# Kernel tuning notes

Measured on AMD Instinct MI355X. Metric: run time of the kernel, lower is better.

The kernel has to match this reference:

```python
import jax, jax.numpy as jnp
import numpy as np

E, H, I, K, T = 8, 1024, 2816, 2, 2048


def setup_inputs() -> dict:
    key = jax.random.key(0)
    k1, k2, k3, k4, k5, k6 = jax.random.split(key, 6)
    hidden_states = jax.random.normal(k1, (T, H), dtype=jnp.float32)
    top_k_indices = jax.random.randint(k2, (T, K), 0, E, dtype=jnp.int32)
    raw = jax.random.uniform(k3, (T, K), dtype=jnp.float32) + 0.1
    top_k_values = raw / jnp.sum(raw, axis=-1, keepdims=True)  # router softmax-like weights
    scale = 1.0 / np.sqrt(H)
    w_gate = jax.random.normal(k4, (E, H, I), dtype=jnp.float32) * scale
    w_up = jax.random.normal(k5, (E, H, I), dtype=jnp.float32) * scale
    w_down = jax.random.normal(k6, (E, I, H), dtype=jnp.float32) * (1.0 / np.sqrt(I))
    return {
        "hidden_states": hidden_states,
        "top_k_indices": top_k_indices,
        "top_k_values": top_k_values,
        "w_gate": w_gate,
        "w_up": w_up,
        "w_down": w_down,
    }


def reference(hidden_states, top_k_indices, top_k_values, w_gate, w_up, w_down):
    # Each expert: SwiGLU FFN  down( silu(x @ gate) * (x @ up) )
    # Run every expert on every token (dense reference for grouped-GEMM dispatch),
    # then combine with the per-token top-k routing weights.
    def expert(wg, wu, wd):
        g = jnp.matmul(hidden_states, wg)          # [T, I]
        u = jnp.matmul(hidden_states, wu)          # [T, I]
        return jnp.matmul(jax.nn.silu(g) * u, wd)  # [T, H]

    y = jax.vmap(expert)(w_gate, w_up, w_down)     # [E, T, H]

    t = hidden_states.shape[0]
    # comb[t, e] = sum over k of top_k_values[t, k] where top_k_indices[t, k] == e
    comb = jnp.zeros((t, w_gate.shape[0]), dtype=hidden_states.dtype)
    comb = comb.at[jnp.arange(t)[:, None], top_k_indices].add(top_k_values)
    out = jnp.einsum('te,eth->th', comb, y)        # weighted combine -> [T, H]
    return out
```

## Files before the change

### kernel.cpp

```cpp
#include <hip/hip_runtime.h>
#include <stdint.h>

#define T_TOK 2048
#define KTOP  2
#define NEXP  8
#define HDIM  1024
#define IDIM  2816

#define NPAIR 4096

#define BM        128
#define MAX_TILES 40
#define NPP       (NPAIR + BM)
#define BN2       128
#define BK2       32
#define BN3       64
#define BK3       64

#define R1BM   256
#define R1T    24
#define R1NPP  (NPAIR + R1BM)
#define R1BN2  128
#define R1BK2  32
#define R1BKp2 40
#define R1BN3  64
#define R1BK3  64
#define R1BKp3 72

typedef __attribute__((ext_vector_type(8))) short short8;
typedef __attribute__((ext_vector_type(4))) float floatx4;

__device__ __forceinline__ unsigned short f2bf(float f) {
  unsigned int u = __float_as_uint(f);
  u += 0x7fffu + ((u >> 16) & 1u);
  return (unsigned short)(u >> 16);
}

__device__ __forceinline__ void glds16(const unsigned short* g, unsigned short* l) {
  __builtin_amdgcn_global_load_lds(
      (const __attribute__((address_space(1))) unsigned int*)g,
      (__attribute__((address_space(3))) unsigned int*)l, 16, 0, 0);
}

__global__ void setup_kernel(const int* __restrict__ idx,
                             const float* __restrict__ vals,
                             int* __restrict__ hdr,
                             int* __restrict__ stok,
                             float* __restrict__ sw, int bm) {
  __shared__ int cnt[NEXP];
  __shared__ int off[NEXP];
  int tid = threadIdx.x;
  if (tid < NEXP) cnt[tid] = 0;
  __syncthreads();
  for (int p = tid; p < NPAIR; p += blockDim.x) atomicAdd(&cnt[idx[p]], 1);
  __syncthreads();
  if (tid == 0) {
    int s = 0, nt = 0;
    for (int e = 0; e < NEXP; ++e) {
      off[e] = s;
      int n = cnt[e];
      for (int t0 = 0; t0 < n; t0 += bm) {
        hdr[nt] = e;
        hdr[64 + nt] = s + t0;
        hdr[128 + nt] = s + n;
        nt++;
      }
      s += n;
    }
    for (; nt < 64; ++nt) hdr[nt] = -1;
  }
  __syncthreads();
  for (int p = tid; p < NPAIR; p += blockDim.x) {
    int e = idx[p];
    int pos = atomicAdd(&off[e], 1);
    stok[pos] = p / KTOP;
    sw[pos] = vals[p];
  }
}

__global__ void gather_kernel(const float* __restrict__ hidden,
                              const int* __restrict__ stok,
                              unsigned short* __restrict__ Xs) {
  int p = blockIdx.x;
  int t = stok[p];
  const float4* src = reinterpret_cast<const float4*>(hidden + (size_t)t * HDIM);
  float4 v = src[threadIdx.x];
  uint2 q;
  q.x = f2bf(v.x) | ((unsigned)f2bf(v.y) << 16);
  q.y = f2bf(v.z) | ((unsigned)f2bf(v.w) << 16);
  *reinterpret_cast<uint2*>(Xs + (size_t)p * HDIM + threadIdx.x * 4) = q;
}

__global__ __launch_bounds__(256) void convert_kernel(
    const float* __restrict__ wg, const float* __restrict__ wu,
    const float* __restrict__ wd, unsigned short* __restrict__ wgT,
    unsigned short* __restrict__ wuT, unsigned short* __restrict__ wdT,
    int zoff) {
  __shared__ float ls[64][65];
  int z = blockIdx.z + zoff;
  int e = blockIdx.y;
  int M = (z == 2) ? IDIM : HDIM;
  int N = (z == 2) ? HDIM : IDIM;
  const float* src = (z == 0 ? wg : z == 1 ? wu : wd) + (size_t)e * M * N;
  unsigned short* dst = (z == 0 ? wgT : z == 1 ? wuT : wdT) + (size_t)e * M * N;
  int ntx = N >> 6;
  int n0 = (blockIdx.x % ntx) << 6;
  int m0 = (blockIdx.x / ntx) << 6;
  int t = threadIdx.x;
  int rr = t >> 4, cc = (t & 15) * 4;
#pragma unroll
  for (int i = 0; i < 4; ++i) {
    int r = rr + i * 16;
    float4 v = *reinterpret_cast<const float4*>(src + (size_t)(m0 + r) * N + n0 + cc);
    ls[r][cc] = v.x; ls[r][cc + 1] = v.y; ls[r][cc + 2] = v.z; ls[r][cc + 3] = v.w;
  }
  __syncthreads();
  int mc = (t & 7) * 8, nn = t >> 3;
#pragma unroll
  for (int i = 0; i < 2; ++i) {
    int n = nn + i * 32;
    uint4 q;
    q.x = f2bf(ls[mc][n])     | ((unsigned)f2bf(ls[mc + 1][n]) << 16);
    q.y = f2bf(ls[mc + 2][n]) | ((unsigned)f2bf(ls[mc + 3][n]) << 16);
    q.z = f2bf(ls[mc + 4][n]) | ((unsigned)f2bf(ls[mc + 5][n]) << 16);
    q.w = f2bf(ls[mc + 6][n]) | ((unsigned)f2bf(ls[mc + 7][n]) << 16);
    *reinterpret_cast<uint4*>(dst + (size_t)(n0 + n) * M + m0 + mc) = q;
  }
}

__global__ __launch_bounds__(256, 2) void gateup_kernel(
    const unsigned short* __restrict__ Xs, const unsigned short* __restrict__ wgT,
    const unsigned short* __restrict__ wuT, const int* __restrict__ hdr,
    const float* __restrict__ sw_g, unsigned short* __restrict__ Act) {
  int bx = blockIdx.x;
  int e = hdr[bx];
  if (e < 0) return;
  int row0 = hdr[64 + bx];
  int rowlim = hdr[128 + bx] - row0;
  int n0 = blockIdx.y * BN2;

  __shared__ __align__(16) unsigned short As[BM * BK2];
  __shared__ __align__(16) unsigned short Bg[BN2 * BK2];
  __shared__ __align__(16) unsigned short Bu[BN2 * BK2];
  __shared__ float sw[BM];

  int tid = threadIdx.x, lane = tid & 63, wave = tid >> 6;
  if (tid < BM) sw[tid] = sw_g[row0 + tid];

  const unsigned short* wgb = wgT + (size_t)e * IDIM * HDIM;
  const unsigned short* wub = wuT + (size_t)e * IDIM * HDIM;

  floatx4 accg[4][4], accu[4][4];
  floatx4 zz = {0.f, 0.f, 0.f, 0.f};
#pragma unroll
  for (int a = 0; a < 4; ++a)
#pragma unroll
    for (int b = 0; b < 4; ++b) { accg[a][b] = zz; accu[a][b] = zz; }

  int wm = (wave >> 1) * 64, wn = (wave & 1) * 64;
  int lr = lane >> 2;
  int lk = (((lane & 3) ^ ((lr >> 1) & 3)) * 8);
  int fr = lane & 15;
  int fq = (((lane >> 4) ^ ((fr >> 1) & 3)) * 8);

  for (int kb = 0; kb < HDIM; kb += BK2) {
#pragma unroll
    for (int it = 0; it < 2; ++it) {
      int c = wave * 2 + it;
      glds16(Xs  + (size_t)(row0 + c * 16 + lr) * HDIM + kb + lk, &As[c * 512]);
      glds16(wgb + (size_t)(n0  + c * 16 + lr) * HDIM + kb + lk, &Bg[c * 512]);
      glds16(wub + (size_t)(n0  + c * 16 + lr) * HDIM + kb + lk, &Bu[c * 512]);
    }
    __syncthreads();

    short8 af[4], bg8[4], bu8[4];
#pragma unroll
    for (int x = 0; x < 4; ++x) {
      af[x]  = *reinterpret_cast<const short8*>(&As[(wm + x * 16 + fr) * BK2 + fq]);
      bg8[x] = *reinterpret_cast<const short8*>(&Bg[(wn + x * 16 + fr) * BK2 + fq]);
      bu8[x] = *reinterpret_cast<const short8*>(&Bu[(wn + x * 16 + fr) * BK2 + fq]);
    }
#pragma unroll
    for (int tm = 0; tm < 4; ++tm)
#pragma unroll
      for (int tn = 0; tn < 4; ++tn) {
        accg[tm][tn] = __builtin_amdgcn_mfma_f32_16x16x32_bf16(af[tm], bg8[tn], accg[tm][tn], 0, 0, 0);
        accu[tm][tn] = __builtin_amdgcn_mfma_f32_16x16x32_bf16(af[tm], bu8[tn], accu[tm][tn], 0, 0, 0);
      }
    __syncthreads();
  }

#pragma unroll
  for (int tm = 0; tm < 4; ++tm)
#pragma unroll
    for (int tn = 0; tn < 4; ++tn)
#pragma unroll
      for (int r = 0; r < 4; ++r) {
        int rl = wm + tm * 16 + (lane >> 4) * 4 + r;
        if (rl < rowlim) {
          int col = n0 + wn + tn * 16 + fr;
          float g = accg[tm][tn][r];
          float u = accu[tm][tn][r];
          float s = g / (1.f + __expf(-g));
          Act[(size_t)(row0 + rl) * IDIM + col] = f2bf(s * u * sw[rl]);
        }
      }
}

__global__ __launch_bounds__(256, 3) void down_kernel(
    const unsigned short* __restrict__ Act, const unsigned short* __restrict__ wdT,
    const int* __restrict__ hdr, const int* __restrict__ stok,
    float* __restrict__ out) {
  int bx = blockIdx.x;
  int e = hdr[bx];
  if (e < 0) return;
  int row0 = hdr[64 + bx];
  int rowlim = hdr[128 + bx] - row0;
  int n0 = blockIdx.y * BN3;

  __shared__ __align__(16) unsigned short As[BM * BK3];
  __shared__ __align__(16) unsigned short Bd[BN3 * BK3];
  __shared__ int stk[BM];

  int tid = threadIdx.x, lane = tid & 63, wave = tid >> 6;
  if (tid < BM) stk[tid] = stok[row0 + tid];

  const unsigned short* wdb = wdT + (size_t)e * HDIM * IDIM;

  floatx4 acc[4][2];
  floatx4 zz = {0.f, 0.f, 0.f, 0.f};
#pragma unroll
  for (int a = 0; a < 4; ++a) { acc[a][0] = zz; acc[a][1] = zz; }

  int wm = (wave >> 1) * 64, wn = (wave & 1) * 32;
  int lr8 = lane >> 3;
  int lk8 = (((lane & 7) ^ lr8) * 8);
  int fr = lane & 15;
  int fk = fr & 7;

  for (int kb = 0; kb < IDIM; kb += BK3) {
#pragma unroll
    for (int it = 0; it < 4; ++it) {
      int c = wave * 4 + it;
      glds16(Act + (size_t)(row0 + c * 8 + lr8) * IDIM + kb + lk8, &As[c * 512]);
    }
#pragma unroll
    for (int it = 0; it < 2; ++it) {
      int c = wave * 2 + it;
      glds16(wdb + (size_t)(n0 + c * 8 + lr8) * IDIM + kb + lk8, &Bd[c * 512]);
    }
    __syncthreads();

#pragma unroll
    for (int ks = 0; ks < BK3; ks += 32) {
      int q8 = (ks >> 3) + (lane >> 4);
      int fo = ((q8 ^ fk) * 8);
      short8 af[4], bd8[2];
#pragma unroll
      for (int x = 0; x < 4; ++x)
        af[x] = *reinterpret_cast<const short8*>(&As[(wm + x * 16 + fr) * BK3 + fo]);
#pragma unroll
      for (int x = 0; x < 2; ++x)
        bd8[x] = *reinterpret_cast<const short8*>(&Bd[(wn + x * 16 + fr) * BK3 + fo]);
#pragma unroll
      for (int tm = 0; tm < 4; ++tm)
#pragma unroll
        for (int tn = 0; tn < 2; ++tn)
          acc[tm][tn] = __builtin_amdgcn_mfma_f32_16x16x32_bf16(af[tm], bd8[tn], acc[tm][tn], 0, 0, 0);
    }
    __syncthreads();
  }

#pragma unroll
  for (int tm = 0; tm < 4; ++tm)
#pragma unroll
    for (int tn = 0; tn < 2; ++tn)
#pragma unroll
      for (int r = 0; r < 4; ++r) {
        int rl = wm + tm * 16 + (lane >> 4) * 4 + r;
        if (rl < rowlim) {
          int col = n0 + wn + tn * 16 + fr;
          unsafeAtomicAdd(&out[(size_t)stk[rl] * HDIM + col], acc[tm][tn][r]);
        }
      }
}

__global__ __launch_bounds__(512, 2) void gateup_fb(
    const unsigned short* __restrict__ Xs, const float* __restrict__ wg,
    const float* __restrict__ wu, const int* __restrict__ hdr,
    const float* __restrict__ sw_g, unsigned short* __restrict__ Act) {
  int by = blockIdx.y;
  int e = hdr[by];
  if (e < 0) return;
  int row0 = hdr[64 + by];
  int row_end = hdr[128 + by];
  int n0 = blockIdx.x * R1BN2;

  __shared__ __align__(16) unsigned short As[R1BM * R1BKp2];
  __shared__ __align__(16) unsigned short Bg[R1BN2 * R1BKp2];
  __shared__ __align__(16) unsigned short Bu[R1BN2 * R1BKp2];
  __shared__ float sw[R1BM];

  int tid = threadIdx.x, lane = tid & 63, wave = tid >> 6;
  if (tid < R1BM) sw[tid] = sw_g[row0 + tid];

  const float* wgb = wg + (size_t)e * HDIM * IDIM;
  const float* wub = wu + (size_t)e * HDIM * IDIM;

  floatx4 accg[4][4], accu[4][4];
  floatx4 zz = {0.f, 0.f, 0.f, 0.f};
#pragma unroll
  for (int a = 0; a < 4; ++a)
#pragma unroll
    for (int b = 0; b < 4; ++b) { accg[a][b] = zz; accu[a][b] = zz; }

  int wm = (wave >> 1) * 64, wn = (wave & 1) * 64;

  for (int kb = 0; kb < HDIM; kb += R1BK2) {
    __syncthreads();
#pragma unroll
    for (int it = 0; it < 2; ++it) {
      int cc = wave * 2 + it;
      int m = cc * 16 + (lane >> 2);
      int k = (lane & 3) * 8;
      uint4 v = *reinterpret_cast<const uint4*>(Xs + (size_t)(row0 + m) * HDIM + kb + k);
      *reinterpret_cast<uint4*>(&As[m * R1BKp2 + k]) = v;
    }
#pragma unroll
    for (int it = 0; it < 2; ++it) {
      int cc = wave * 2 + it;
      const float* wb = (cc & 8) ? wub : wgb;
      unsigned short* Bs = (cc & 8) ? Bu : Bg;
      int r = cc & 7;
      int kblk = r >> 1, nh = r & 1;
      int n = nh * 64 + lane;
      int k = kblk * 8;
      const float* src = wb + (size_t)(kb + k) * IDIM + n0 + n;
      uint4 q;
      q.x = f2bf(src[0])                | ((unsigned)f2bf(src[(size_t)IDIM])     << 16);
      q.y = f2bf(src[2 * (size_t)IDIM]) | ((unsigned)f2bf(src[3 * (size_t)IDIM]) << 16);
      q.z = f2bf(src[4 * (size_t)IDIM]) | ((unsigned)f2bf(src[5 * (size_t)IDIM]) << 16);
      q.w = f2bf(src[6 * (size_t)IDIM]) | ((unsigned)f2bf(src[7 * (size_t)IDIM]) << 16);
      *reinterpret_cast<uint4*>(&Bs[n * R1BKp2 + k]) = q;
    }
    __syncthreads();

    int krd = (lane >> 4) * 8;
    short8 af[4], bgf[4], buf_[4];
#pragma unroll
    for (int tm = 0; tm < 4; ++tm)
      af[tm] = *reinterpret_cast<const short8*>(&As[(wm + tm * 16 + (lane & 15)) * R1BKp2 + krd]);
#pragma unroll
    for (int tn = 0; tn < 4; ++tn) {
      bgf[tn]  = *reinterpret_cast<const short8*>(&Bg[(wn + tn * 16 + (lane & 15)) * R1BKp2 + krd]);
      buf_[tn] = *reinterpret_cast<const short8*>(&Bu[(wn + tn * 16 + (lane & 15)) * R1BKp2 + krd]);
    }
#pragma unroll
    for (int tm = 0; tm < 4; ++tm)
#pragma unroll
      for (int tn = 0; tn < 4; ++tn) {
        accg[tm][tn] = __builtin_amdgcn_mfma_f32_16x16x32_bf16(af[tm], bgf[tn], accg[tm][tn], 0, 0, 0);
        accu[tm][tn] = __builtin_amdgcn_mfma_f32_16x16x32_bf16(af[tm], buf_[tn], accu[tm][tn], 0, 0, 0);
      }
  }

  int rowlim = row_end - row0;
#pragma unroll
  for (int tm = 0; tm < 4; ++tm)
#pragma unroll
    for (int tn = 0; tn < 4; ++tn)
#pragma unroll
      for (int r = 0; r < 4; ++r) {
        int rl = wm + tm * 16 + (lane >> 4) * 4 + r;
        if (rl < rowlim) {
          int col = n0 + wn + tn * 16 + (lane & 15);
          float g = accg[tm][tn][r];
          float u = accu[tm][tn][r];
          float s = g / (1.f + __expf(-g));
          Act[(size_t)(row0 + rl) * IDIM + col] = f2bf(s * u * sw[rl]);
        }
      }
}

__global__ __launch_bounds__(512, 2) void down_fb(
    const unsigned short* __restrict__ Act, const float* __restrict__ wd,
    const int* __restrict__ hdr, const int* __restrict__ stok,
    float* __restrict__ out) {
  int by = blockIdx.y;
  int e = hdr[by];
  if (e < 0) return;
  int row0 = hdr[64 + by];
  int row_end = hdr[128 + by];
  int n0 = blockIdx.x * R1BN3;

  __shared__ __align__(16) unsigned short As[R1BM * R1BKp3];
  __shared__ __align__(16) unsigned short Bd[R1BN3 * R1BKp3];
  __shared__ int stk[R1BM];

  int tid = threadIdx.x, lane = tid & 63, wave = tid >> 6;
  if (tid < R1BM) stk[tid] = stok[row0 + tid];

  const float* wdb = wd + (size_t)e * IDIM * HDIM;

  floatx4 acc[4][2];
  floatx4 zz = {0.f, 0.f, 0.f, 0.f};
#pragma unroll
  for (int a = 0; a < 4; ++a) { acc[a][0] = zz; acc[a][1] = zz; }

  int wm = (wave >> 1) * 64, wn = (wave & 1) * 32;

  for (int kb = 0; kb < IDIM; kb += R1BK3) {
    __syncthreads();
#pragma unroll
    for (int it = 0; it < 4; ++it) {
      int cc = wave * 4 + it;
      int m = cc * 8 + (lane >> 3);
      int k = (lane & 7) * 8;
      uint4 v = *reinterpret_cast<const uint4*>(Act + (size_t)(row0 + m) * IDIM + kb + k);
      *reinterpret_cast<uint4*>(&As[m * R1BKp3 + k]) = v;
    }
    {
      int n = lane;
      int k = wave * 8;
      const float* src = wdb + (size_t)(kb + k) * HDIM + n0 + n;
      uint4 q;
      q.x = f2bf(src[0])        | ((unsigned)f2bf(src[HDIM])     << 16);
      q.y = f2bf(src[2 * HDIM]) | ((unsigned)f2bf(src[3 * HDIM]) << 16);
      q.z = f2bf(src[4 * HDIM]) | ((unsigned)f2bf(src[5 * HDIM]) << 16);
      q.w = f2bf(src[6 * HDIM]) | ((unsigned)f2bf(src[7 * HDIM]) << 16);
      *reinterpret_cast<uint4*>(&Bd[n * R1BKp3 + k]) = q;
    }
    __syncthreads();

#pragma unroll
    for (int ks = 0; ks < R1BK3; ks += 32) {
      int krd = ks + (lane >> 4) * 8;
      short8 af[4], bdf[2];
#pragma unroll
      for (int tm = 0; tm < 4; ++tm)
        af[tm] = *reinterpret_cast<const short8*>(&As[(wm + tm * 16 + (lane & 15)) * R1BKp3 + krd]);
#pragma unroll
      for (int tn = 0; tn < 2; ++tn)
        bdf[tn] = *reinterpret_cast<const short8*>(&Bd[(wn + tn * 16 + (lane & 15)) * R1BKp3 + krd]);
#pragma unroll
      for (int tm = 0; tm < 4; ++tm)
#pragma unroll
        for (int tn = 0; tn < 2; ++tn)
          acc[tm][tn] = __builtin_amdgcn_mfma_f32_16x16x32_bf16(af[tm], bdf[tn], acc[tm][tn], 0, 0, 0);
    }
  }

  int rowlim = row_end - row0;
#pragma unroll
  for (int tm = 0; tm < 4; ++tm)
#pragma unroll
    for (int tn = 0; tn < 2; ++tn)
#pragma unroll
      for (int r = 0; r < 4; ++r) {
        int rl = wm + tm * 16 + (lane >> 4) * 4 + r;
        if (rl < rowlim) {
          int col = n0 + wn + tn * 16 + (lane & 15);
          unsafeAtomicAdd(&out[(size_t)stk[rl] * HDIM + col], acc[tm][tn][r]);
        }
      }
}

extern "C" void kernel_launch(void* const* d_in, const int* in_sizes, int n_in,
                              void* d_out, int out_size, void* d_ws, size_t ws_size,
                              hipStream_t stream) {
  const float* hidden = (const float*)d_in[0];
  const int* idx = (const int*)d_in[1];
  const float* vals = (const float*)d_in[2];
  const float* wg = (const float*)d_in[3];
  const float* wu = (const float*)d_in[4];
  const float* wd = (const float*)d_in[5];
  float* out = (float*)d_out;
  char* ws = (char*)d_ws;

  hipMemsetAsync(d_out, 0, (size_t)out_size * sizeof(float), stream);

  const size_t OFF_STOK = 4096;
  const size_t OFF_SW   = OFF_STOK + (size_t)NPP * 4;
  const size_t OFF_XS   = 65536;
  const size_t OFF_ACT  = OFF_XS + (size_t)NPP * HDIM * 2;
  const size_t OFF_WG   = OFF_ACT + (size_t)NPP * IDIM * 2;
  const size_t WSZ      = (size_t)NEXP * HDIM * IDIM * 2;
  const size_t OFF_WU   = OFF_WG + WSZ;
  const size_t NEED     = OFF_WU + WSZ;

  if (ws_size >= NEED) {
    int* hdr = (int*)ws;
    int* stok = (int*)(ws + OFF_STOK);
    float* sw = (float*)(ws + OFF_SW);
    unsigned short* Xs  = (unsigned short*)(ws + OFF_XS);
    unsigned short* Act = (unsigned short*)(ws + OFF_ACT);
    unsigned short* wgT = (unsigned short*)(ws + OFF_WG);
    unsigned short* wuT = (unsigned short*)(ws + OFF_WU);
    unsigned short* wdT = wgT;

    setup_kernel<<<1, 256, 0, stream>>>(idx, vals, hdr, stok, sw, BM);
    convert_kernel<<<dim3(704, NEXP, 2), 256, 0, stream>>>(wg, wu, wd, wgT, wuT, wdT, 0);
    gather_kernel<<<NPAIR, 256, 0, stream>>>(hidden, stok, Xs);
    gateup_kernel<<<dim3(MAX_TILES, IDIM / BN2), 256, 0, stream>>>(Xs, wgT, wuT, hdr, sw, Act);
    convert_kernel<<<dim3(704, NEXP, 1), 256, 0, stream>>>(wg, wu, wd, wgT, wuT, wdT, 2);
    down_kernel<<<dim3(MAX_TILES, HDIM / BN3), 256, 0, stream>>>(Act, wdT, hdr, stok, out);
  } else {
    int* hdr = (int*)ws;
    int* stok = (int*)(ws + 4096);
    float* sw = (float*)(ws + 4096 + (size_t)R1NPP * 4);
    unsigned short* Xs  = (unsigned short*)(ws + 65536);
    unsigned short* Act = (unsigned short*)(ws + 65536 + (size_t)R1NPP * HDIM * 2);

    setup_kernel<<<1, 256, 0, stream>>>(idx, vals, hdr, stok, sw, R1BM);
    gather_kernel<<<NPAIR, 256, 0, stream>>>(hidden, stok, Xs);
    gateup_fb<<<dim3(IDIM / R1BN2, R1T), 512, 0, stream>>>(Xs, wg, wu, hdr, sw, Act);
    down_fb<<<dim3(HDIM / R1BN3, R1T), 512, 0, stream>>>(Act, wd, hdr, stok, out);
  }
}
```

Baseline: 451.8 us.

## Double-buffer LDS in grouped GEMMs, remap tiles across XCDs, use packed bf16 convert

The gate/up and down GEMM kernels now double-buffer their LDS tiles, issuing the async global-to-LDS load for the next K block before computing on the current one. This is meant to overlap memory latency with MFMA work. The expert tile index is permuted so consecutive block IDs spread across the XCDs. The scalar bf16 rounding is replaced with the v_cvt_pk_bf16_f32 instruction in gather and convert, and the setup kernel launches with 1024 threads. Double buffering doubles LDS use per block, which may lower occupancy against the declared launch bounds.

```diff
diff --git a/kernel.cpp b/kernel.cpp
--- a/kernel.cpp
+++ b/kernel.cpp
@@ -36,10 +36,20 @@
   return (unsigned short)(u >> 16);
 }
 
+__device__ __forceinline__ unsigned int pkbf(float a, float b) {
+  unsigned int r;
+  asm volatile("v_cvt_pk_bf16_f32 %0, %1, %2" : "=v"(r) : "v"(a), "v"(b));
+  return r;
+}
+
 __device__ __forceinline__ void glds16(const unsigned short* g, unsigned short* l) {
   __builtin_amdgcn_global_load_lds(
       (const __attribute__((address_space(1))) unsigned int*)g,
       (__attribute__((address_space(3))) unsigned int*)l, 16, 0, 0);
+}
+
+__device__ __forceinline__ int xcd_tile(int bx0) {
+  return (bx0 & 7) * (MAX_TILES / 8) + (bx0 >> 3);
 }
 
 __global__ void setup_kernel(const int* __restrict__ idx,
@@ -86,8 +96,8 @@
   const float4* src = reinterpret_cast<const float4*>(hidden + (size_t)t * HDIM);
   float4 v = src[threadIdx.x];
   uint2 q;
-  q.x = f2bf(v.x) | ((unsigned)f2bf(v.y) << 16);
-  q.y = f2bf(v.z) | ((unsigned)f2bf(v.w) << 16);
+  q.x = pkbf(v.x, v.y);
+  q.y = pkbf(v.z, v.w);
   *reinterpret_cast<uint2*>(Xs + (size_t)p * HDIM + threadIdx.x * 4) = q;
 }
 
@@ -120,11 +130,24 @@
   for (int i = 0; i < 2; ++i) {
     int n = nn + i * 32;
     uint4 q;
-    q.x = f2bf(ls[mc][n])     | ((unsigned)f2bf(ls[mc + 1][n]) << 16);
-    q.y = f2bf(ls[mc + 2][n]) | ((unsigned)f2bf(ls[mc + 3][n]) << 16);
-    q.z = f2bf(ls[mc + 4][n]) | ((unsigned)f2bf(ls[mc + 5][n]) << 16);
-    q.w = f2bf(ls[mc + 6][n]) | ((unsigned)f2bf(ls[mc + 7][n]) << 16);
+    q.x = pkbf(ls[mc][n],     ls[mc + 1][n]);
+    q.y = pkbf(ls[mc + 2][n], ls[mc + 3][n]);
+    q.z = pkbf(ls[mc + 4][n], ls[mc + 5][n]);
+    q.w = pkbf(ls[mc + 6][n], ls[mc + 7][n]);
     *reinterpret_cast<uint4*>(dst + (size_t)(n0 + n) * M + m0 + mc) = q;
+  }
+}
+
+__device__ __forceinline__ void stage_gu(
+    const unsigned short* __restrict__ Xs, const unsigned short* __restrict__ wgb,
+    const unsigned short* __restrict__ wub, int row0, int n0, int wave, int lr,
+    int lk, int kb, unsigned short* As, unsigned short* Bg, unsigned short* Bu) {
+#pragma unroll
+  for (int it = 0; it < 2; ++it) {
+    int c = wave * 2 + it;
+    glds16(Xs  + (size_t)(row0 + c * 16 + lr) * HDIM + kb + lk, &As[c * 512]);
+    glds16(wgb + (size_t)(n0  + c * 16 + lr) * HDIM + kb + lk, &Bg[c * 512]);
+    glds16(wub + (size_t)(n0  + c * 16 + lr) * HDIM + kb + lk, &Bu[c * 512]);
   }
 }
 
@@ -132,16 +155,16 @@
     const unsigned short* __restrict__ Xs, const unsigned short* __restrict__ wgT,
     const unsigned short* __restrict__ wuT, const int* __restrict__ hdr,
     const float* __restrict__ sw_g, unsigned short* __restrict__ Act) {
-  int bx = blockIdx.x;
+  int bx = xcd_tile(blockIdx.x);
   int e = hdr[bx];
   if (e < 0) return;
   int row0 = hdr[64 + bx];
   int rowlim = hdr[128 + bx] - row0;
   int n0 = blockIdx.y * BN2;
 
-  __shared__ __align__(16) unsigned short As[BM * BK2];
-  __shared__ __align__(16) unsigned short Bg[BN2 * BK2];
-  __shared__ __align__(16) unsigned short Bu[BN2 * BK2];
+  __shared__ __align__(16) unsigned short As[2][BM * BK2];
+  __shared__ __align__(16) unsigned short Bg[2][BN2 * BK2];
+  __shared__ __align__(16) unsigned short Bu[2][BN2 * BK2];
   __shared__ float sw[BM];
 
   int tid = threadIdx.x, lane = tid & 63, wave = tid >> 6;
@@ -163,22 +186,24 @@
   int fr = lane & 15;
   int fq = (((lane >> 4) ^ ((fr >> 1) & 3)) * 8);
 
+  stage_gu(Xs, wgb, wub, row0, n0, wave, lr, lk, 0, As[0], Bg[0], Bu[0]);
+  __syncthreads();
+
+  int cur = 0;
   for (int kb = 0; kb < HDIM; kb += BK2) {
-#pragma unroll
-    for (int it = 0; it < 2; ++it) {
-      int c = wave * 2 + it;
-      glds16(Xs  + (size_t)(row0 + c * 16 + lr) * HDIM + kb + lk, &As[c * 512]);
-      glds16(wgb + (size_t)(n0  + c * 16 + lr) * HDIM + kb + lk, &Bg[c * 512]);
-      glds16(wub + (size_t)(n0  + c * 16 + lr) * HDIM + kb + lk, &Bu[c * 512]);
-    }
-    __syncthreads();
-
+    if (kb + BK2 < HDIM)
+      stage_gu(Xs, wgb, wub, row0, n0, wave, lr, lk, kb + BK2,
+               As[cur ^ 1], Bg[cur ^ 1], Bu[cur ^ 1]);
+
+    const unsigned short* Asc = As[cur];
+    const unsigned short* Bgc = Bg[cur];
+    const unsigned short* Buc = Bu[cur];
     short8 af[4], bg8[4], bu8[4];
 #pragma unroll
     for (int x = 0; x < 4; ++x) {
-      af[x]  = *reinterpret_cast<const short8*>(&As[(wm + x * 16 + fr) * BK2 + fq]);
-      bg8[x] = *reinterpret_cast<const short8*>(&Bg[(wn + x * 16 + fr) * BK2 + fq]);
-      bu8[x] = *reinterpret_cast<const short8*>(&Bu[(wn + x * 16 + fr) * BK2 + fq]);
+      af[x]  = *reinterpret_cast<const short8*>(&Asc[(wm + x * 16 + fr) * BK2 + fq]);
+      bg8[x] = *reinterpret_cast<const short8*>(&Bgc[(wn + x * 16 + fr) * BK2 + fq]);
+      bu8[x] = *reinterpret_cast<const short8*>(&Buc[(wn + x * 16 + fr) * BK2 + fq]);
     }
 #pragma unroll
     for (int tm = 0; tm < 4; ++tm)
@@ -188,6 +213,7 @@
         accu[tm][tn] = __builtin_amdgcn_mfma_f32_16x16x32_bf16(af[tm], bu8[tn], accu[tm][tn], 0, 0, 0);
       }
     __syncthreads();
+    cur ^= 1;
   }
 
 #pragma unroll
@@ -207,19 +233,35 @@
       }
 }
 
+__device__ __forceinline__ void stage_dn(
+    const unsigned short* __restrict__ Act, const unsigned short* __restrict__ wdb,
+    int row0, int n0, int wave, int lr8, int lk8, int kb,
+    unsigned short* As, unsigned short* Bd) {
+#pragma unroll
+  for (int it = 0; it < 4; ++it) {
+    int c = wave * 4 + it;
+    glds16(Act + (size_t)(row0 + c * 8 + lr8) * IDIM + kb + lk8, &As[c * 512]);
+  }
+#pragma unroll
+  for (int it = 0; it < 2; ++it) {
+    int c = wave * 2 + it;
+    glds16(wdb + (size_t)(n0 + c * 8 + lr8) * IDIM + kb + lk8, &Bd[c * 512]);
+  }
+}
+
 __global__ __launch_bounds__(256, 3) void down_kernel(
     const unsigned short* __restrict__ Act, const unsigned short* __restrict__ wdT,
     const int* __restrict__ hdr, const int* __restrict__ stok,
     float* __restrict__ out) {
-  int bx = blockIdx.x;
+  int bx = xcd_tile(blockIdx.x);
   int e = hdr[bx];
   if (e < 0) return;
   int row0 = hdr[64 + bx];
   int rowlim = hdr[128 + bx] - row0;
   int n0 = blockIdx.y * BN3;
 
-  __shared__ __align__(16) unsigned short As[BM * BK3];
-  __shared__ __align__(16) unsigned short Bd[BN3 * BK3];
+  __shared__ __align__(16) unsigned short As[2][BM * BK3];
+  __shared__ __align__(16) unsigned short Bd[2][BN3 * BK3];
   __shared__ int stk[BM];
 
   int tid = threadIdx.x, lane = tid & 63, wave = tid >> 6;
@@ -238,19 +280,16 @@
   int fr = lane & 15;
   int fk = fr & 7;
 
+  stage_dn(Act, wdb, row0, n0, wave, lr8, lk8, 0, As[0], Bd[0]);
+  __syncthreads();
+
+  int cur = 0;
   for (int kb = 0; kb < IDIM; kb += BK3) {
-#pragma unroll
-    for (int it = 0; it < 4; ++it) {
-      int c = wave * 4 + it;
-      glds16(Act + (size_t)(row0 + c * 8 + lr8) * IDIM + kb + lk8, &As[c * 512]);
-    }
-#pragma unroll
-    for (int it = 0; it < 2; ++it) {
-      int c = wave * 2 + it;
-      glds16(wdb + (size_t)(n0 + c * 8 + lr8) * IDIM + kb + lk8, &Bd[c * 512]);
-    }
-    __syncthreads();
-
+    if (kb + BK3 < IDIM)
+      stage_dn(Act, wdb, row0, n0, wave, lr8, lk8, kb + BK3, As[cur ^ 1], Bd[cur ^ 1]);
+
+    const unsigned short* Asc = As[cur];
+    const unsigned short* Bdc = Bd[cur];
 #pragma unroll
     for (int ks = 0; ks < BK3; ks += 32) {
       int q8 = (ks >> 3) + (lane >> 4);
@@ -258,10 +297,10 @@
       short8 af[4], bd8[2];
 #pragma unroll
       for (int x = 0; x < 4; ++x)
-        af[x] = *reinterpret_cast<const short8*>(&As[(wm + x * 16 + fr) * BK3 + fo]);
+        af[x] = *reinterpret_cast<const short8*>(&Asc[(wm + x * 16 + fr) * BK3 + fo]);
 #pragma unroll
       for (int x = 0; x < 2; ++x)
-        bd8[x] = *reinterpret_cast<const short8*>(&Bd[(wn + x * 16 + fr) * BK3 + fo]);
+        bd8[x] = *reinterpret_cast<const short8*>(&Bdc[(wn + x * 16 + fr) * BK3 + fo]);
 #pragma unroll
       for (int tm = 0; tm < 4; ++tm)
 #pragma unroll
@@ -269,6 +308,7 @@
           acc[tm][tn] = __builtin_amdgcn_mfma_f32_16x16x32_bf16(af[tm], bd8[tn], acc[tm][tn], 0, 0, 0);
     }
     __syncthreads();
+    cur ^= 1;
   }
 
 #pragma unroll
@@ -498,7 +538,7 @@
     unsigned short* wuT = (unsigned short*)(ws + OFF_WU);
     unsigned short* wdT = wgT;
 
-    setup_kernel<<<1, 256, 0, stream>>>(idx, vals, hdr, stok, sw, BM);
+    setup_kernel<<<1, 1024, 0, stream>>>(idx, vals, hdr, stok, sw, BM);
     convert_kernel<<<dim3(704, NEXP, 2), 256, 0, stream>>>(wg, wu, wd, wgT, wuT, wdT, 0);
     gather_kernel<<<NPAIR, 256, 0, stream>>>(hidden, stok, Xs);
     gateup_kernel<<<dim3(MAX_TILES, IDIM / BN2), 256, 0, stream>>>(Xs, wgT, wuT, hdr, sw, Act);
@@ -511,7 +551,7 @@
     unsigned short* Xs  = (unsigned short*)(ws + 65536);
     unsigned short* Act = (unsigned short*)(ws + 65536 + (size_t)R1NPP * HDIM * 2);
 
-    setup_kernel<<<1, 256, 0, stream>>>(idx, vals, hdr, stok, sw, R1BM);
+    setup_kernel<<<1, 1024, 0, stream>>>(idx, vals, hdr, stok, sw, R1BM);
     gather_kernel<<<NPAIR, 256, 0, stream>>>(hidden, stok, Xs);
     gateup_fb<<<dim3(IDIM / R1BN2, R1T), 512, 0, stream>>>(Xs, wg, wu, hdr, sw, Act);
     down_fb<<<dim3(HDIM / R1BN3, R1T), 512, 0, stream>>>(Act, wd, hdr, stok, out);
```

New measurement: 435.5 us. 1.04x faster.
